# Kernel optimization log

Measured on AMD Instinct MI355X. Metric: run time of the kernel, lower is better.

Reference implementation:

```python
import jax, jax.numpy as jnp
import numpy as np

L2 = (0.01, 0.01)
L1_RATIO = 0.5
EPS = 1e-16


def soft_thresholding(x, t):
    return jnp.sign(x) * jnp.maximum(jnp.abs(x) - t, 0.0)


def update_u(x, u, v, l1, l2, eps=EPS):
    # x: [B,M,N], u: [B,M,R], v: [B,N,R]
    a = jnp.einsum('bmn,bnr->bmr', x, v)      # x @ v            [B,M,R]
    b = jnp.einsum('bnr,bns->brs', v, v)      # v.mT @ v         [B,R,R]
    R = u.shape[-1]

    def step(u_new, r):
        # Gauss-Seidel update of column r using the freshest u_new (sequential dependency)
        br = jnp.take(b, r, axis=-1)                        # b[..., :, r]   [B,R]
        brr = jnp.take(br, r, axis=-1)                      # b[..., r, r]   [B]
        # term2 = u_new[..., indices] @ b[..., indices, r] computed as full matvec minus the r-th term
        term2 = jnp.einsum('bmk,bk->bm', u_new, br) - jnp.take(u_new, r, axis=-1) * brr[:, None]
        num = soft_thresholding(jnp.take(a, r, axis=-1) - term2, l1)   # [B,M]
        den = brr[:, None] + l2                                        # [B,1]
        ur = (num + eps) / (den + eps)
        return u_new.at[..., r].set(ur), None

    u_new, _ = jax.lax.scan(step, u, jnp.arange(R))
    return u_new


def setup_inputs() -> dict:
    key = jax.random.key(0)
    k1, k2, k3 = jax.random.split(key, 3)
    B, M, N, R = 8, 2048, 2048, 32
    x = jax.random.normal(k1, (B, M, N), dtype=jnp.float32)
    u = jax.random.normal(k2, (B, M, R), dtype=jnp.float32)
    v = jax.random.normal(k3, (B, N, R), dtype=jnp.float32)
    return {"x": x, "u": u, "v": v}


def reference(x, u, v):
    M, N = x.shape[-2], x.shape[-1]
    l1_u = L2[0] * L1_RATIO * N
    l2_u = L2[0] * (1.0 - L1_RATIO) * N
    l1_v = L2[1] * L1_RATIO * M
    l2_v = L2[1] * (1.0 - L1_RATIO) * M
    u = update_u(x, u, v, l1_u, l2_u)                              # factor 0
    v = update_u(jnp.swapaxes(x, -1, -2), v, u, l1_v, l2_v)        # factor 1 (update_v)
    return (u, v)
```

## Files before the change

### kernel.cpp

```cpp
#include <hip/hip_runtime.h>
#include <hip/hip_bf16.h>

#define NB 8
#define MD 2048
#define RD 32
#define KSPLIT 4
#define KSL (2048 / KSPLIT)
#define VT_STRIDE 520
#define XT_STRIDE 40

typedef float floatx4 __attribute__((ext_vector_type(4)));
typedef short shortx8 __attribute__((ext_vector_type(8)));

static __device__ __forceinline__ short f2b(float f) {
    __hip_bfloat16 h = __float2bfloat16(f);
    return (short)*reinterpret_cast<unsigned short*>(&h);
}

__global__ __launch_bounds__(256) void bmat_kernel(const float* __restrict__ w,
                                                   float* __restrict__ bmat) {
    int batch = blockIdx.x >> 5;
    int n0 = (blockIdx.x & 31) * 64;
    int t = threadIdx.x;
    __shared__ float ws[64][36];
    const float* wb = w + ((size_t)batch * 2048 + n0) * RD;
#pragma unroll
    for (int i = 0; i < 8; ++i) {
        int idx = t + i * 256;
        ws[idx >> 5][idx & 31] = wb[(idx >> 5) * RD + (idx & 31)];
    }
    __syncthreads();
    int ii = t >> 3;
    int jq = (t & 7) * 4;
    float acc[4] = {0.f, 0.f, 0.f, 0.f};
    for (int n = 0; n < 64; ++n) {
        float wi = ws[n][ii];
        float4 wj = *(const float4*)&ws[n][jq];
        acc[0] = fmaf(wi, wj.x, acc[0]);
        acc[1] = fmaf(wi, wj.y, acc[1]);
        acc[2] = fmaf(wi, wj.z, acc[2]);
        acc[3] = fmaf(wi, wj.w, acc[3]);
    }
    float* bp = bmat + ((size_t)batch * RD + ii) * RD + jq;
#pragma unroll
    for (int c = 0; c < 4; ++c) atomicAdd(bp + c, acc[c]);
}

__global__ __launch_bounds__(256, 4) void gemm1_kernel(const float* __restrict__ x,
                                                       const float* __restrict__ v,
                                                       float* __restrict__ a) {
    __shared__ short wT[32 * VT_STRIDE];
    int bz = blockIdx.x;
    int ks = bz & (KSPLIT - 1);
    int mblk = (bz >> 2) & 31;
    int batch = bz >> 7;
    int t = threadIdx.x;
    int lane = t & 63;
    int wave = t >> 6;

    const float* wb = v + ((size_t)batch * 2048 + ks * KSL) * RD;
#pragma unroll
    for (int i = 0; i < 16; ++i) {
        int idx = t + i * 256;
        int k = idx >> 3;
        int rq = (idx & 7) * 4;
        float4 f = *(const float4*)(wb + (size_t)k * RD + rq);
        wT[(rq + 0) * VT_STRIDE + k] = f2b(f.x);
        wT[(rq + 1) * VT_STRIDE + k] = f2b(f.y);
        wT[(rq + 2) * VT_STRIDE + k] = f2b(f.z);
        wT[(rq + 3) * VT_STRIDE + k] = f2b(f.w);
    }
    __syncthreads();

    int kq = (lane >> 4) * 8;
    const float* xrow =
        x + ((size_t)batch * MD + mblk * 64 + wave * 16 + (lane & 15)) * 2048 + ks * KSL + kq;
    int r0 = (lane & 15) * VT_STRIDE + kq;
    int r1 = ((lane & 15) + 16) * VT_STRIDE + kq;

    floatx4 acc0 = {0.f, 0.f, 0.f, 0.f}, acc1 = {0.f, 0.f, 0.f, 0.f};
    float4 fa = *(const float4*)(xrow);
    float4 fb = *(const float4*)(xrow + 4);
    for (int s = 0; s < KSL / 32; ++s) {
        float4 na = {0, 0, 0, 0}, nb = {0, 0, 0, 0};
        if (s + 1 < KSL / 32) {
            na = *(const float4*)(xrow + (s + 1) * 32);
            nb = *(const float4*)(xrow + (s + 1) * 32 + 4);
        }
        shortx8 af = {f2b(fa.x), f2b(fa.y), f2b(fa.z), f2b(fa.w),
                      f2b(fb.x), f2b(fb.y), f2b(fb.z), f2b(fb.w)};
        shortx8 b0 = *(const shortx8*)&wT[r0 + s * 32];
        shortx8 b1 = *(const shortx8*)&wT[r1 + s * 32];
        acc0 = __builtin_amdgcn_mfma_f32_16x16x32_bf16(af, b0, acc0, 0, 0, 0);
        acc1 = __builtin_amdgcn_mfma_f32_16x16x32_bf16(af, b1, acc1, 0, 0, 0);
        fa = na;
        fb = nb;
    }
    float* ab = a + ((size_t)batch * 2048 + mblk * 64 + wave * 16 + (lane >> 4) * 4) * RD + (lane & 15);
#pragma unroll
    for (int i = 0; i < 4; ++i) {
        atomicAdd(ab + i * RD, acc0[i]);
        atomicAdd(ab + i * RD + 16, acc1[i]);
    }
}

__global__ __launch_bounds__(256, 4) void gemm2_kernel(const float* __restrict__ x,
                                                       const float* __restrict__ u,
                                                       float* __restrict__ a) {
    __shared__ short uT[32 * VT_STRIDE];
    __shared__ short xT[4 * 16 * XT_STRIDE];
    int bz = blockIdx.x;
    int ks = bz & (KSPLIT - 1);
    int nblk = (bz >> 2) & 31;
    int batch = bz >> 7;
    int t = threadIdx.x;
    int lane = t & 63;
    int wave = t >> 6;

    const float* ub = u + ((size_t)batch * 2048 + ks * KSL) * RD;
#pragma unroll
    for (int i = 0; i < 16; ++i) {
        int idx = t + i * 256;
        int k = idx >> 3;
        int rq = (idx & 7) * 4;
        float4 f = *(const float4*)(ub + (size_t)k * RD + rq);
        uT[(rq + 0) * VT_STRIDE + k] = f2b(f.x);
        uT[(rq + 1) * VT_STRIDE + k] = f2b(f.y);
        uT[(rq + 2) * VT_STRIDE + k] = f2b(f.z);
        uT[(rq + 3) * VT_STRIDE + k] = f2b(f.w);
    }
    __syncthreads();

    short* xTw = &xT[wave * 16 * XT_STRIDE];
    int mloc = lane & 31;
    int ng = (lane >> 5) * 8;
    int n0w = nblk * 64 + wave * 16;
    const float* xp = x + ((size_t)batch * 2048 + ks * KSL + mloc) * 2048 + n0w + ng;

    int nl = lane & 15;
    int kq = (lane >> 4) * 8;
    int rA = nl * XT_STRIDE + kq;
    int rB0 = nl * VT_STRIDE + kq;
    int rB1 = (nl + 16) * VT_STRIDE + kq;

    floatx4 acc0 = {0.f, 0.f, 0.f, 0.f}, acc1 = {0.f, 0.f, 0.f, 0.f};
    float4 fa = *(const float4*)xp;
    float4 fb = *(const float4*)(xp + 4);
    for (int s = 0; s < KSL / 32; ++s) {
        xTw[(ng + 0) * XT_STRIDE + mloc] = f2b(fa.x);
        xTw[(ng + 1) * XT_STRIDE + mloc] = f2b(fa.y);
        xTw[(ng + 2) * XT_STRIDE + mloc] = f2b(fa.z);
        xTw[(ng + 3) * XT_STRIDE + mloc] = f2b(fa.w);
        xTw[(ng + 4) * XT_STRIDE + mloc] = f2b(fb.x);
        xTw[(ng + 5) * XT_STRIDE + mloc] = f2b(fb.y);
        xTw[(ng + 6) * XT_STRIDE + mloc] = f2b(fb.z);
        xTw[(ng + 7) * XT_STRIDE + mloc] = f2b(fb.w);
        float4 na = {0, 0, 0, 0}, nb = {0, 0, 0, 0};
        if (s + 1 < KSL / 32) {
            na = *(const float4*)(xp + (size_t)(s + 1) * 32 * 2048);
            nb = *(const float4*)(xp + (size_t)(s + 1) * 32 * 2048 + 4);
        }
        shortx8 af = *(const shortx8*)&xTw[rA];
        shortx8 b0 = *(const shortx8*)&uT[rB0 + s * 32];
        shortx8 b1 = *(const shortx8*)&uT[rB1 + s * 32];
        acc0 = __builtin_amdgcn_mfma_f32_16x16x32_bf16(af, b0, acc0, 0, 0, 0);
        acc1 = __builtin_amdgcn_mfma_f32_16x16x32_bf16(af, b1, acc1, 0, 0, 0);
        fa = na;
        fb = nb;
    }
    float* ab = a + ((size_t)batch * 2048 + n0w + (lane >> 4) * 4) * RD + (lane & 15);
#pragma unroll
    for (int i = 0; i < 4; ++i) {
        atomicAdd(ab + i * RD, acc0[i]);
        atomicAdd(ab + i * RD + 16, acc1[i]);
    }
}

__global__ __launch_bounds__(256) void gs_kernel(const float* __restrict__ uin,
                                                 const float* __restrict__ amat,
                                                 const float* __restrict__ bmat,
                                                 float* __restrict__ uout,
                                                 float l1, float l2) {
    int blk = blockIdx.x;
    int batch = blk >> 3;
    int m = (blk & 7) * 256 + threadIdx.x;
    __shared__ float bs[RD][RD];
    ((float4*)&bs[0][0])[threadIdx.x] =
        ((const float4*)(bmat + (size_t)batch * RD * RD))[threadIdx.x];
    __syncthreads();
    float uv[RD], av[RD];
    const float* up = uin + ((size_t)batch * 2048 + m) * RD;
    const float* ap = amat + ((size_t)batch * 2048 + m) * RD;
#pragma unroll
    for (int q = 0; q < 8; ++q) {
        *(float4*)&uv[q * 4] = *(const float4*)&up[q * 4];
        *(float4*)&av[q * 4] = *(const float4*)&ap[q * 4];
    }
#pragma unroll
    for (int r = 0; r < RD; ++r) {
        float brr = bs[r][r];
        float t2 = -uv[r] * brr;
#pragma unroll
        for (int k = 0; k < RD; ++k) t2 = fmaf(uv[k], bs[r][k], t2);
        float num = av[r] - t2;
        float mag = fmaxf(fabsf(num) - l1, 0.f);
        num = copysignf(mag, num);
        uv[r] = (num + 1e-16f) / (brr + l2 + 1e-16f);
    }
    float* op = uout + ((size_t)batch * 2048 + m) * RD;
#pragma unroll
    for (int q = 0; q < 8; ++q) *(float4*)&op[q * 4] = *(float4*)&uv[q * 4];
}

extern "C" void kernel_launch(void* const* d_in, const int* in_sizes, int n_in,
                              void* d_out, int out_size, void* d_ws, size_t ws_size,
                              hipStream_t stream) {
    const float* x = (const float*)d_in[0];
    const float* u = (const float*)d_in[1];
    const float* v = (const float*)d_in[2];
    float* out_u = (float*)d_out;
    float* out_v = out_u + (size_t)NB * MD * RD;
    float* a_ws = (float*)d_ws;
    float* b_ws = a_ws + (size_t)NB * 2048 * RD;
    const float l1u = 10.24f, l2u = 10.24f;
    const float l1v = 10.24f, l2v = 10.24f;
    size_t abytes = (size_t)NB * 2048 * RD * sizeof(float);
    size_t bbytes = (size_t)NB * RD * RD * sizeof(float);

    hipMemsetAsync(a_ws, 0, abytes + bbytes, stream);
    bmat_kernel<<<NB * 32, 256, 0, stream>>>(v, b_ws);
    gemm1_kernel<<<NB * 32 * KSPLIT, 256, 0, stream>>>(x, v, a_ws);
    gs_kernel<<<NB * 8, 256, 0, stream>>>(u, a_ws, b_ws, out_u, l1u, l2u);

    hipMemsetAsync(a_ws, 0, abytes + bbytes, stream);
    bmat_kernel<<<NB * 32, 256, 0, stream>>>(out_u, b_ws);
    gemm2_kernel<<<NB * 32 * KSPLIT, 256, 0, stream>>>(x, out_u, a_ws);
    gs_kernel<<<NB * 8, 256, 0, stream>>>(v, a_ws, b_ws, out_v, l1v, l2v);
}
```

Before: 257.4 us.

## Fuse Gram computation into GEMM, replace atomics with split-K partial buffers

Merges the two GEMM kernels into one templated kernel and folds the Gram-matrix (w^T w) computation into the ks==0 blocks, which removes the separate bmat launches. The atomicAdd accumulation and the memsets are replaced by plain stores to per-split partial buffers, which the Gauss-Seidel kernel sums on load. The shared-memory layout for the bf16 weight tile is reordered so each lane reads a contiguous 8-element fragment. This trades fewer launches and no atomics for extra partial-buffer traffic, and the launch-bounds occupancy hint is dropped because of the larger LDS allocation.

```diff
diff --git a/kernel.cpp b/kernel.cpp
--- a/kernel.cpp
+++ b/kernel.cpp
@@ -1,13 +1,9 @@
 #include <hip/hip_runtime.h>
 #include <hip/hip_bf16.h>
 
-#define NB 8
-#define MD 2048
-#define RD 32
+#define L1REG 10.24f
+#define L2REG 10.24f
 #define KSPLIT 4
-#define KSL (2048 / KSPLIT)
-#define VT_STRIDE 520
-#define XT_STRIDE 40
 
 typedef float floatx4 __attribute__((ext_vector_type(4)));
 typedef short shortx8 __attribute__((ext_vector_type(8)));
@@ -17,199 +13,164 @@
     return (short)*reinterpret_cast<unsigned short*>(&h);
 }
 
-__global__ __launch_bounds__(256) void bmat_kernel(const float* __restrict__ w,
-                                                   float* __restrict__ bmat) {
-    int batch = blockIdx.x >> 5;
-    int n0 = (blockIdx.x & 31) * 64;
-    int t = threadIdx.x;
-    __shared__ float ws[64][36];
-    const float* wb = w + ((size_t)batch * 2048 + n0) * RD;
-#pragma unroll
-    for (int i = 0; i < 8; ++i) {
-        int idx = t + i * 256;
-        ws[idx >> 5][idx & 31] = wb[(idx >> 5) * RD + (idx & 31)];
-    }
-    __syncthreads();
-    int ii = t >> 3;
-    int jq = (t & 7) * 4;
-    float acc[4] = {0.f, 0.f, 0.f, 0.f};
-    for (int n = 0; n < 64; ++n) {
-        float wi = ws[n][ii];
-        float4 wj = *(const float4*)&ws[n][jq];
-        acc[0] = fmaf(wi, wj.x, acc[0]);
-        acc[1] = fmaf(wi, wj.y, acc[1]);
-        acc[2] = fmaf(wi, wj.z, acc[2]);
-        acc[3] = fmaf(wi, wj.w, acc[3]);
-    }
-    float* bp = bmat + ((size_t)batch * RD + ii) * RD + jq;
-#pragma unroll
-    for (int c = 0; c < 4; ++c) atomicAdd(bp + c, acc[c]);
-}
+template <bool TRANS>
+__global__ __launch_bounds__(256) void gemm_kernel(const float* __restrict__ x,
+                                                   const float* __restrict__ w,
+                                                   float* __restrict__ ap,
+                                                   float* __restrict__ pb) {
+    __shared__ __align__(16) short bf[16384];
+    __shared__ __align__(16) short xT[2048];
+    int bz = blockIdx.x, t = threadIdx.x;
+    int batch = bz >> 7, mblk = (bz >> 2) & 31, ks = bz & 3;
 
-__global__ __launch_bounds__(256, 4) void gemm1_kernel(const float* __restrict__ x,
-                                                       const float* __restrict__ v,
-                                                       float* __restrict__ a) {
-    __shared__ short wT[32 * VT_STRIDE];
-    int bz = blockIdx.x;
-    int ks = bz & (KSPLIT - 1);
-    int mblk = (bz >> 2) & 31;
-    int batch = bz >> 7;
-    int t = threadIdx.x;
-    int lane = t & 63;
-    int wave = t >> 6;
-
-    const float* wb = v + ((size_t)batch * 2048 + ks * KSL) * RD;
+    const float* wsrc = w + ((size_t)batch * 2048 + ks * 512) * 32;
 #pragma unroll
     for (int i = 0; i < 16; ++i) {
         int idx = t + i * 256;
         int k = idx >> 3;
         int rq = (idx & 7) * 4;
-        float4 f = *(const float4*)(wb + (size_t)k * RD + rq);
-        wT[(rq + 0) * VT_STRIDE + k] = f2b(f.x);
-        wT[(rq + 1) * VT_STRIDE + k] = f2b(f.y);
-        wT[(rq + 2) * VT_STRIDE + k] = f2b(f.z);
-        wT[(rq + 3) * VT_STRIDE + k] = f2b(f.w);
+        float4 f = *(const float4*)(wsrc + (size_t)k * 32 + rq);
+        int sbase = (k >> 5) * 512 + ((k >> 3) & 3) * 128 + (k & 7);
+        float fv[4] = {f.x, f.y, f.z, f.w};
+#pragma unroll
+        for (int c = 0; c < 4; ++c) {
+            int r = rq + c;
+            bf[(r >> 4) * 8192 + sbase + (r & 15) * 8] = f2b(fv[c]);
+        }
     }
     __syncthreads();
 
-    int kq = (lane >> 4) * 8;
-    const float* xrow =
-        x + ((size_t)batch * MD + mblk * 64 + wave * 16 + (lane & 15)) * 2048 + ks * KSL + kq;
-    int r0 = (lane & 15) * VT_STRIDE + kq;
-    int r1 = ((lane & 15) + 16) * VT_STRIDE + kq;
+    int lane = t & 63, wave = t >> 6;
+    int b0off = lane * 8;
+    floatx4 acc0 = {0.f, 0.f, 0.f, 0.f}, acc1 = {0.f, 0.f, 0.f, 0.f};
 
-    floatx4 acc0 = {0.f, 0.f, 0.f, 0.f}, acc1 = {0.f, 0.f, 0.f, 0.f};
-    float4 fa = *(const float4*)(xrow);
-    float4 fb = *(const float4*)(xrow + 4);
-    for (int s = 0; s < KSL / 32; ++s) {
-        float4 na = {0, 0, 0, 0}, nb = {0, 0, 0, 0};
-        if (s + 1 < KSL / 32) {
-            na = *(const float4*)(xrow + (s + 1) * 32);
-            nb = *(const float4*)(xrow + (s + 1) * 32 + 4);
+    if (!TRANS) {
+        int kq = (lane >> 4) * 8;
+        const float* xrow =
+            x + ((size_t)batch * 2048 + mblk * 64 + wave * 16 + (lane & 15)) * 2048 + ks * 512 + kq;
+        float4 fa = *(const float4*)xrow;
+        float4 fb = *(const float4*)(xrow + 4);
+#pragma unroll
+        for (int s = 0; s < 16; ++s) {
+            float4 na = {0, 0, 0, 0}, nb = {0, 0, 0, 0};
+            if (s < 15) {
+                na = *(const float4*)(xrow + (s + 1) * 32);
+                nb = *(const float4*)(xrow + (s + 1) * 32 + 4);
+            }
+            shortx8 af = {f2b(fa.x), f2b(fa.y), f2b(fa.z), f2b(fa.w),
+                          f2b(fb.x), f2b(fb.y), f2b(fb.z), f2b(fb.w)};
+            shortx8 b0 = *(const shortx8*)&bf[s * 512 + b0off];
+            shortx8 b1 = *(const shortx8*)&bf[8192 + s * 512 + b0off];
+            acc0 = __builtin_amdgcn_mfma_f32_16x16x32_bf16(af, b0, acc0, 0, 0, 0);
+            acc1 = __builtin_amdgcn_mfma_f32_16x16x32_bf16(af, b1, acc1, 0, 0, 0);
+            fa = na;
+            fb = nb;
         }
-        shortx8 af = {f2b(fa.x), f2b(fa.y), f2b(fa.z), f2b(fa.w),
-                      f2b(fb.x), f2b(fb.y), f2b(fb.z), f2b(fb.w)};
-        shortx8 b0 = *(const shortx8*)&wT[r0 + s * 32];
-        shortx8 b1 = *(const shortx8*)&wT[r1 + s * 32];
-        acc0 = __builtin_amdgcn_mfma_f32_16x16x32_bf16(af, b0, acc0, 0, 0, 0);
-        acc1 = __builtin_amdgcn_mfma_f32_16x16x32_bf16(af, b1, acc1, 0, 0, 0);
-        fa = na;
-        fb = nb;
+    } else {
+        short* xTw = &xT[wave * 512];
+        int mloc = lane & 31;
+        int ng = (lane >> 5) * 8;
+        int n0w = mblk * 64 + wave * 16;
+        const float* xp = x + ((size_t)batch * 2048 + ks * 512 + mloc) * 2048 + n0w + ng;
+        int rA = (lane & 15) * 32 + (lane >> 4) * 8;
+        float4 fa = *(const float4*)xp;
+        float4 fb = *(const float4*)(xp + 4);
+#pragma unroll
+        for (int s = 0; s < 16; ++s) {
+            xTw[(ng + 0) * 32 + mloc] = f2b(fa.x);
+            xTw[(ng + 1) * 32 + mloc] = f2b(fa.y);
+            xTw[(ng + 2) * 32 + mloc] = f2b(fa.z);
+            xTw[(ng + 3) * 32 + mloc] = f2b(fa.w);
+            xTw[(ng + 4) * 32 + mloc] = f2b(fb.x);
+            xTw[(ng + 5) * 32 + mloc] = f2b(fb.y);
+            xTw[(ng + 6) * 32 + mloc] = f2b(fb.z);
+            xTw[(ng + 7) * 32 + mloc] = f2b(fb.w);
+            float4 na = {0, 0, 0, 0}, nb = {0, 0, 0, 0};
+            if (s < 15) {
+                na = *(const float4*)(xp + (size_t)(s + 1) * 32 * 2048);
+                nb = *(const float4*)(xp + (size_t)(s + 1) * 32 * 2048 + 4);
+            }
+            shortx8 af = *(const shortx8*)&xTw[rA];
+            shortx8 b0 = *(const shortx8*)&bf[s * 512 + b0off];
+            shortx8 b1 = *(const shortx8*)&bf[8192 + s * 512 + b0off];
+            acc0 = __builtin_amdgcn_mfma_f32_16x16x32_bf16(af, b0, acc0, 0, 0, 0);
+            acc1 = __builtin_amdgcn_mfma_f32_16x16x32_bf16(af, b1, acc1, 0, 0, 0);
+            fa = na;
+            fb = nb;
+        }
     }
-    float* ab = a + ((size_t)batch * 2048 + mblk * 64 + wave * 16 + (lane >> 4) * 4) * RD + (lane & 15);
+    int orow = mblk * 64 + wave * 16 + (lane >> 4) * 4;
+    float* ab = ap + (((size_t)ks * 8 + batch) * 2048 + orow) * 32 + (lane & 15);
 #pragma unroll
     for (int i = 0; i < 4; ++i) {
-        atomicAdd(ab + i * RD, acc0[i]);
-        atomicAdd(ab + i * RD + 16, acc1[i]);
+        ab[i * 32] = acc0[i];
+        ab[i * 32 + 16] = acc1[i];
+    }
+
+    if (ks == 0) {
+        const float* wsl = w + ((size_t)batch * 2048 + mblk * 64) * 32;
+        int ii = t >> 3, jq = (t & 7) * 4;
+        float a0 = 0.f, a1 = 0.f, a2 = 0.f, a3 = 0.f;
+#pragma unroll 8
+        for (int n = 0; n < 64; ++n) {
+            float wi = wsl[n * 32 + ii];
+            float4 wj = *(const float4*)(wsl + n * 32 + jq);
+            a0 = fmaf(wi, wj.x, a0);
+            a1 = fmaf(wi, wj.y, a1);
+            a2 = fmaf(wi, wj.z, a2);
+            a3 = fmaf(wi, wj.w, a3);
+        }
+        float4 res = {a0, a1, a2, a3};
+        *(float4*)(pb + ((size_t)mblk * 8 + batch) * 1024 + ii * 32 + jq) = res;
     }
 }
 
-__global__ __launch_bounds__(256, 4) void gemm2_kernel(const float* __restrict__ x,
-                                                       const float* __restrict__ u,
-                                                       float* __restrict__ a) {
-    __shared__ short uT[32 * VT_STRIDE];
-    __shared__ short xT[4 * 16 * XT_STRIDE];
-    int bz = blockIdx.x;
-    int ks = bz & (KSPLIT - 1);
-    int nblk = (bz >> 2) & 31;
-    int batch = bz >> 7;
-    int t = threadIdx.x;
-    int lane = t & 63;
-    int wave = t >> 6;
-
-    const float* ub = u + ((size_t)batch * 2048 + ks * KSL) * RD;
-#pragma unroll
-    for (int i = 0; i < 16; ++i) {
-        int idx = t + i * 256;
-        int k = idx >> 3;
-        int rq = (idx & 7) * 4;
-        float4 f = *(const float4*)(ub + (size_t)k * RD + rq);
-        uT[(rq + 0) * VT_STRIDE + k] = f2b(f.x);
-        uT[(rq + 1) * VT_STRIDE + k] = f2b(f.y);
-        uT[(rq + 2) * VT_STRIDE + k] = f2b(f.z);
-        uT[(rq + 3) * VT_STRIDE + k] = f2b(f.w);
+__global__ __launch_bounds__(256) void gs_kernel(const float* __restrict__ win,
+                                                 const float* __restrict__ ap,
+                                                 const float* __restrict__ pb,
+                                                 float* __restrict__ wout) {
+    __shared__ float bs[1024];
+    int bz = blockIdx.x, t = threadIdx.x;
+    int batch = bz >> 3;
+    int m = (bz & 7) * 256 + t;
+    float4 bacc = {0.f, 0.f, 0.f, 0.f};
+    const float* pbb = pb + (size_t)batch * 1024 + t * 4;
+#pragma unroll 8
+    for (int s = 0; s < 32; ++s) {
+        float4 p = *(const float4*)(pbb + (size_t)s * 8192);
+        bacc.x += p.x; bacc.y += p.y; bacc.z += p.z; bacc.w += p.w;
     }
+    *(float4*)&bs[t * 4] = bacc;
     __syncthreads();
 
-    short* xTw = &xT[wave * 16 * XT_STRIDE];
-    int mloc = lane & 31;
-    int ng = (lane >> 5) * 8;
-    int n0w = nblk * 64 + wave * 16;
-    const float* xp = x + ((size_t)batch * 2048 + ks * KSL + mloc) * 2048 + n0w + ng;
-
-    int nl = lane & 15;
-    int kq = (lane >> 4) * 8;
-    int rA = nl * XT_STRIDE + kq;
-    int rB0 = nl * VT_STRIDE + kq;
-    int rB1 = (nl + 16) * VT_STRIDE + kq;
-
-    floatx4 acc0 = {0.f, 0.f, 0.f, 0.f}, acc1 = {0.f, 0.f, 0.f, 0.f};
-    float4 fa = *(const float4*)xp;
-    float4 fb = *(const float4*)(xp + 4);
-    for (int s = 0; s < KSL / 32; ++s) {
-        xTw[(ng + 0) * XT_STRIDE + mloc] = f2b(fa.x);
-        xTw[(ng + 1) * XT_STRIDE + mloc] = f2b(fa.y);
-        xTw[(ng + 2) * XT_STRIDE + mloc] = f2b(fa.z);
-        xTw[(ng + 3) * XT_STRIDE + mloc] = f2b(fa.w);
-        xTw[(ng + 4) * XT_STRIDE + mloc] = f2b(fb.x);
-        xTw[(ng + 5) * XT_STRIDE + mloc] = f2b(fb.y);
-        xTw[(ng + 6) * XT_STRIDE + mloc] = f2b(fb.z);
-        xTw[(ng + 7) * XT_STRIDE + mloc] = f2b(fb.w);
-        float4 na = {0, 0, 0, 0}, nb = {0, 0, 0, 0};
-        if (s + 1 < KSL / 32) {
-            na = *(const float4*)(xp + (size_t)(s + 1) * 32 * 2048);
-            nb = *(const float4*)(xp + (size_t)(s + 1) * 32 * 2048 + 4);
-        }
-        shortx8 af = *(const shortx8*)&xTw[rA];
-        shortx8 b0 = *(const shortx8*)&uT[rB0 + s * 32];
-        shortx8 b1 = *(const shortx8*)&uT[rB1 + s * 32];
-        acc0 = __builtin_amdgcn_mfma_f32_16x16x32_bf16(af, b0, acc0, 0, 0, 0);
-        acc1 = __builtin_amdgcn_mfma_f32_16x16x32_bf16(af, b1, acc1, 0, 0, 0);
-        fa = na;
-        fb = nb;
-    }
-    float* ab = a + ((size_t)batch * 2048 + n0w + (lane >> 4) * 4) * RD + (lane & 15);
+    float uv[32], av[32];
+    const float* up = win + ((size_t)batch * 2048 + m) * 32;
 #pragma unroll
-    for (int i = 0; i < 4; ++i) {
-        atomicAdd(ab + i * RD, acc0[i]);
-        atomicAdd(ab + i * RD + 16, acc1[i]);
-    }
-}
-
-__global__ __launch_bounds__(256) void gs_kernel(const float* __restrict__ uin,
-                                                 const float* __restrict__ amat,
-                                                 const float* __restrict__ bmat,
-                                                 float* __restrict__ uout,
-                                                 float l1, float l2) {
-    int blk = blockIdx.x;
-    int batch = blk >> 3;
-    int m = (blk & 7) * 256 + threadIdx.x;
-    __shared__ float bs[RD][RD];
-    ((float4*)&bs[0][0])[threadIdx.x] =
-        ((const float4*)(bmat + (size_t)batch * RD * RD))[threadIdx.x];
-    __syncthreads();
-    float uv[RD], av[RD];
-    const float* up = uin + ((size_t)batch * 2048 + m) * RD;
-    const float* ap = amat + ((size_t)batch * 2048 + m) * RD;
+    for (int q = 0; q < 8; ++q) *(float4*)&uv[q * 4] = *(const float4*)(up + q * 4);
 #pragma unroll
     for (int q = 0; q < 8; ++q) {
-        *(float4*)&uv[q * 4] = *(const float4*)&up[q * 4];
-        *(float4*)&av[q * 4] = *(const float4*)&ap[q * 4];
+        float4 sacc = {0.f, 0.f, 0.f, 0.f};
+#pragma unroll
+        for (int ks = 0; ks < KSPLIT; ++ks) {
+            float4 p = *(const float4*)(ap + (((size_t)ks * 8 + batch) * 2048 + m) * 32 + q * 4);
+            sacc.x += p.x; sacc.y += p.y; sacc.z += p.z; sacc.w += p.w;
+        }
+        *(float4*)&av[q * 4] = sacc;
     }
 #pragma unroll
-    for (int r = 0; r < RD; ++r) {
-        float brr = bs[r][r];
+    for (int r = 0; r < 32; ++r) {
+        float brr = bs[r * 32 + r];
         float t2 = -uv[r] * brr;
 #pragma unroll
-        for (int k = 0; k < RD; ++k) t2 = fmaf(uv[k], bs[r][k], t2);
+        for (int k = 0; k < 32; ++k) t2 = fmaf(uv[k], bs[r * 32 + k], t2);
         float num = av[r] - t2;
-        float mag = fmaxf(fabsf(num) - l1, 0.f);
+        float mag = fmaxf(fabsf(num) - L1REG, 0.f);
         num = copysignf(mag, num);
-        uv[r] = (num + 1e-16f) / (brr + l2 + 1e-16f);
+        uv[r] = (num + 1e-16f) / (brr + L2REG + 1e-16f);
     }
-    float* op = uout + ((size_t)batch * 2048 + m) * RD;
+    float* op = wout + ((size_t)batch * 2048 + m) * 32;
 #pragma unroll
-    for (int q = 0; q < 8; ++q) *(float4*)&op[q * 4] = *(float4*)&uv[q * 4];
+    for (int q = 0; q < 8; ++q) *(float4*)(op + q * 4) = *(const float4*)&uv[q * 4];
 }
 
 extern "C" void kernel_launch(void* const* d_in, const int* in_sizes, int n_in,
@@ -219,21 +180,12 @@
     const float* u = (const float*)d_in[1];
     const float* v = (const float*)d_in[2];
     float* out_u = (float*)d_out;
-    float* out_v = out_u + (size_t)NB * MD * RD;
-    float* a_ws = (float*)d_ws;
-    float* b_ws = a_ws + (size_t)NB * 2048 * RD;
-    const float l1u = 10.24f, l2u = 10.24f;
-    const float l1v = 10.24f, l2v = 10.24f;
-    size_t abytes = (size_t)NB * 2048 * RD * sizeof(float);
-    size_t bbytes = (size_t)NB * RD * RD * sizeof(float);
+    float* out_v = out_u + (size_t)8 * 2048 * 32;
+    float* ap = (float*)d_ws;
+    float* pb = ap + (size_t)KSPLIT * 8 * 2048 * 32;
 
-    hipMemsetAsync(a_ws, 0, abytes + bbytes, stream);
-    bmat_kernel<<<NB * 32, 256, 0, stream>>>(v, b_ws);
-    gemm1_kernel<<<NB * 32 * KSPLIT, 256, 0, stream>>>(x, v, a_ws);
-    gs_kernel<<<NB * 8, 256, 0, stream>>>(u, a_ws, b_ws, out_u, l1u, l2u);
-
-    hipMemsetAsync(a_ws, 0, abytes + bbytes, stream);
-    bmat_kernel<<<NB * 32, 256, 0, stream>>>(out_u, b_ws);
-    gemm2_kernel<<<NB * 32 * KSPLIT, 256, 0, stream>>>(x, out_u, a_ws);
-    gs_kernel<<<NB * 8, 256, 0, stream>>>(v, a_ws, b_ws, out_v, l1v, l2v);
+    gemm_kernel<false><<<1024, 256, 0, stream>>>(x, v, ap, pb);
+    gs_kernel<<<64, 256, 0, stream>>>(u, ap, pb, out_u);
+    gemm_kernel<true><<<1024, 256, 0, stream>>>(x, out_u, ap, pb);
+    gs_kernel<<<64, 256, 0, stream>>>(v, ap, pb, out_v);
 }
```

Measured after the change: 269.0 us. +4.5%, slower.
